# Optimization experiments

Measured on AMD Instinct MI355X. Metric: run time of the kernel, lower is better.

## Reference

```python
import jax, jax.numpy as jnp
import numpy as np

N = 50000      # nodes
E = 800000     # edges (avg degree 16)
DIN = 128
HID = 128
OUT = 10       # classes
G = 64         # graphs in batch


def setup_inputs() -> dict:
    key = jax.random.key(0)
    ks = jax.random.split(key, 10)
    x = jax.random.normal(ks[0], (N, DIN), dtype=jnp.float32)
    edge_index = jax.random.randint(ks[1], (2, E), 0, N, dtype=jnp.int32)
    edge_weight = jax.random.uniform(ks[2], (E,), dtype=jnp.float32)
    batch = jnp.sort(jax.random.randint(ks[3], (N,), 0, G, dtype=jnp.int32))
    W1 = jax.random.normal(ks[4], (DIN, HID), dtype=jnp.float32) / np.sqrt(DIN)
    b1 = jnp.zeros((HID,), dtype=jnp.float32)
    W2 = jax.random.normal(ks[5], (HID, HID), dtype=jnp.float32) / np.sqrt(HID)
    b2 = jnp.zeros((HID,), dtype=jnp.float32)
    W3 = jax.random.normal(ks[6], (HID, OUT), dtype=jnp.float32) / np.sqrt(HID)
    b3 = jnp.zeros((OUT,), dtype=jnp.float32)
    return {"x": x, "edge_index": edge_index, "edge_weight": edge_weight,
            "batch": batch, "W1": W1, "b1": b1, "W2": W2, "b2": b2,
            "W3": W3, "b3": b3}


def _gcn_norm(edge_index, edge_weight, n_nodes):
    # PyG gcn_norm: add self-loops with weight 1, D^-1/2 (A+I) D^-1/2
    loop = jnp.arange(n_nodes, dtype=edge_index.dtype)
    src = jnp.concatenate([edge_index[0], loop])
    dst = jnp.concatenate([edge_index[1], loop])
    w = jnp.concatenate([edge_weight, jnp.ones((n_nodes,), edge_weight.dtype)])
    deg = jax.ops.segment_sum(w, dst, num_segments=n_nodes)
    dinv = jnp.where(deg > 0, jax.lax.rsqrt(deg), 0.0)
    norm = dinv[src] * w * dinv[dst]
    return src, dst, norm


def _gcn_conv(x, W, b, src, dst, norm, n_nodes):
    h = x @ W                                      # [N, F] dense transform
    msg = norm[:, None] * h[src]                   # gather + scale  [E+N, F]
    out = jax.ops.segment_sum(msg, dst, num_segments=n_nodes)  # scatter-add
    return out + b


def reference(x, edge_index, edge_weight, batch, W1, b1, W2, b2, W3, b3):
    src, dst, norm = _gcn_norm(edge_index, edge_weight, N)
    h = jax.nn.relu(_gcn_conv(x, W1, b1, src, dst, norm, N))
    h = jax.nn.relu(_gcn_conv(h, W2, b2, src, dst, norm, N))
    h = _gcn_conv(h, W3, b3, src, dst, norm, N)    # [N, OUT]
    # global_mean_pool over graph ids
    sums = jax.ops.segment_sum(h, batch, num_segments=G)          # [G, OUT]
    cnts = jax.ops.segment_sum(jnp.ones((N,), h.dtype), batch, num_segments=G)
    pooled = sums / jnp.maximum(cnts, 1.0)[:, None]
    return jax.nn.log_softmax(pooled, axis=1)
```

## Files before the change

### kernel.cpp

```cpp
#include <hip/hip_runtime.h>
#include <math.h>

#define NN 50000
#define EE 800000
#define GG 64
#define FD 128
#define OUTD 10
#define GB 782
#define BB 196
#define NBU 196
#define NBK 128
#define CH 6250

typedef __attribute__((ext_vector_type(8))) short s8v;
typedef __attribute__((ext_vector_type(4))) float f4v;

static __device__ inline unsigned short f2b(float f) {
    unsigned int u = __float_as_uint(f);
    return (unsigned short)((u + 0x7FFFu + ((u >> 16) & 1u)) >> 16);
}


__global__ void k_prep(const float* __restrict__ W1, const float* __restrict__ W2,
                       unsigned short* __restrict__ Wt1, unsigned short* __restrict__ Wt2) {
    int i = blockIdx.x * blockDim.x + threadIdx.x;
    if (i < FD * FD) {
        int nn = i >> 7, k = i & 127;
        Wt1[i] = f2b(W1[k * FD + nn]);
        Wt2[i] = f2b(W2[k * FD + nn]);
    }
}


static __device__ inline void gemm_f32in_body(int bid, const float* __restrict__ A,
        const unsigned short* __restrict__ Wt, unsigned short* __restrict__ out, int n) {
    int tid = threadIdx.x;
    int wave = tid >> 6, lane = tid & 63;
    int quad = lane >> 4, c16 = lane & 15;
    int rowbase = bid * 64 + wave * 16;
    int rowA = rowbase + c16;
    if (rowA >= n) rowA = n - 1;
    f4v acc[8];
    #pragma unroll
    for (int t = 0; t < 8; ++t) acc[t] = (f4v){0.f, 0.f, 0.f, 0.f};
    #pragma unroll
    for (int k0 = 0; k0 < 128; k0 += 32) {
        const float* ap = A + (size_t)rowA * FD + k0 + quad * 8;
        float4 a0 = *(const float4*)ap;
        float4 a1 = *(const float4*)(ap + 4);
        s8v a;
        a[0] = (short)f2b(a0.x); a[1] = (short)f2b(a0.y);
        a[2] = (short)f2b(a0.z); a[3] = (short)f2b(a0.w);
        a[4] = (short)f2b(a1.x); a[5] = (short)f2b(a1.y);
        a[6] = (short)f2b(a1.z); a[7] = (short)f2b(a1.w);
        #pragma unroll
        for (int t = 0; t < 8; ++t) {
            s8v b = *(const s8v*)(Wt + (size_t)(t * 16 + c16) * FD + k0 + quad * 8);
            acc[t] = __builtin_amdgcn_mfma_f32_16x16x32_bf16(a, b, acc[t], 0, 0, 0);
        }
    }
    #pragma unroll
    for (int t = 0; t < 8; ++t) {
        #pragma unroll
        for (int r = 0; r < 4; ++r) {
            int row = rowbase + quad * 4 + r;
            if (row < n) out[(size_t)row * FD + t * 16 + c16] = f2b(acc[t][r]);
        }
    }
}

__global__ __launch_bounds__(256) void k_megaA(const float* __restrict__ x,
        const unsigned short* __restrict__ Wt1, unsigned short* __restrict__ hA,
        const int* __restrict__ dst, int* __restrict__ cnt2d,
        const int* __restrict__ batch, int* __restrict__ gstart) {
    int b = blockIdx.x;
    int tid = threadIdx.x;
    if (b < GB) {
        gemm_f32in_body(b, x, Wt1, hA, NN);
    } else if (b < GB + NBK) {
        __shared__ unsigned hist[NBU];
        int blk = b - GB;
        if (tid < NBU) hist[tid] = 0;
        __syncthreads();
        int e0 = blk * CH;
        for (int e = e0 + tid; e < e0 + CH; e += 256)
            atomicAdd(&hist[(unsigned)dst[e] >> 8], 1u);
        __syncthreads();
        if (tid < NBU) cnt2d[tid * NBK + blk] = (int)hist[tid];
    } else {
        int i = (b - GB - NBK) * 256 + tid;
        if (i < NN) {
            int bb = batch[i];
            int bp = (i == 0) ? -1 : batch[i - 1];
            for (int g = bp + 1; g <= bb; ++g) gstart[g] = i;
            if (i == NN - 1)
                for (int g = bb + 1; g <= GG; ++g) gstart[g] = NN;
        }
    }
}


__global__ __launch_bounds__(256) void k_scatter(const int* __restrict__ src,
        const int* __restrict__ dst, const float* __restrict__ ew,
        const int* __restrict__ cnt2d, int* __restrict__ bbase_g,
        uint2* __restrict__ rec) {
    __shared__ int colsum[NBU];
    __shared__ int ownoff[NBU];
    __shared__ unsigned cur[NBU];
    __shared__ int wtot_s[4];
    int tid = threadIdx.x;
    int blk = blockIdx.x;
    if (tid < NBU) {
        const int* c = cnt2d + tid * NBK;
        int own = 0, tot = 0;
        for (int b = 0; b < NBK; ++b) {
            int t = c[b];
            if (b < blk) own += t;
            tot += t;
        }
        ownoff[tid] = own;
        colsum[tid] = tot;
    }
    __syncthreads();
    {
        int lane = tid & 63, wv = tid >> 6;
        int v = (tid < NBU) ? colsum[tid] : 0;
        int s = v;
        #pragma unroll
        for (int off = 1; off < 64; off <<= 1) {
            int u = __shfl_up(s, off, 64);
            if (lane >= off) s += u;
        }
        if (lane == 63) wtot_s[wv] = s;
        __syncthreads();
        int pre = 0;
        for (int j = 0; j < wv; ++j) pre += wtot_s[j];
        int base = pre + s - v;
        if (tid < NBU) {
            cur[tid] = (unsigned)(base + ownoff[tid]);
            if (blk == 0) bbase_g[tid] = base;
        }
        if (blk == 0 && tid == NBU - 1) bbase_g[NBU] = base + v;
    }
    __syncthreads();
    int e0 = blk * CH;
    for (int e = e0 + tid; e < e0 + CH; e += 256) {
        int d = dst[e];
        unsigned bkt = (unsigned)d >> 8;
        unsigned pos = atomicAdd(&cur[bkt], 1u);
        rec[pos] = make_uint2(((unsigned)(d & 255) << 16) | (unsigned)src[e],
                              __float_as_uint(ew[e]));
    }
}


__global__ __launch_bounds__(1024) void k_rank(const uint2* __restrict__ rec,
        const int* __restrict__ bbase, unsigned short* __restrict__ rankb,
        int* __restrict__ rowptr, float* __restrict__ dinv, uint2* __restrict__ ent) {
    __shared__ unsigned cntS[256];
    __shared__ float wdegS[256];
    __shared__ int wtot_s[4];
    int b = blockIdx.x;
    int tid = threadIdx.x;
    if (tid < 256) { cntS[tid] = 0; wdegS[tid] = 0.0f; }
    __syncthreads();
    int beg = bbase[b], end = bbase[b + 1];
    for (int s = beg + tid; s < end; s += 1024) {
        uint2 r = rec[s];
        unsigned dl = r.x >> 16;
        unsigned old = atomicAdd(&cntS[dl], 1u);
        rankb[s] = (unsigned short)old;
        atomicAdd(&wdegS[dl], __uint_as_float(r.y));
    }
    __syncthreads();
    if (tid < 256) {
        int lane = tid & 63, wv = tid >> 6;
        int v = (int)cntS[tid];
        int s = v;
        #pragma unroll
        for (int off = 1; off < 64; off <<= 1) {
            int u = __shfl_up(s, off, 64);
            if (lane >= off) s += u;
        }
        if (lane == 63) wtot_s[wv] = s;
        __syncthreads();
        int pre = 0;
        for (int j = 0; j < wv; ++j) pre += wtot_s[j];
        int excl = pre + s - v;
        int node = b * 256 + tid;
        if (node < NN) {
            int r = beg + node + excl;
            rowptr[node] = r;
            float di = 1.0f / sqrtf(wdegS[tid] + 1.0f);
            dinv[node] = di;
            ent[r + v] = make_uint2((unsigned)node, __float_as_uint(di * di));
        }
        if (node == NN - 1) rowptr[NN] = EE + NN;
    }
}


__global__ __launch_bounds__(1024) void k_fill2(const uint2* __restrict__ rec,
        const unsigned short* __restrict__ rankb, const int* __restrict__ bbase,
        const int* __restrict__ rowptr, const float* __restrict__ dinv,
        uint2* __restrict__ ent) {
    int b = blockIdx.x;
    int tid = threadIdx.x;
    int beg = bbase[b], end = bbase[b + 1];
    for (int s = beg + tid; s < end; s += 1024) {
        uint2 r = rec[s];
        unsigned sn = r.x & 0xFFFFu;
        int d = (b << 8) | (int)(r.x >> 16);
        int pos = rowptr[d] + (int)rankb[s];
        float val = dinv[sn] * __uint_as_float(r.y) * dinv[d];
        ent[pos] = make_uint2(sn, __float_as_uint(val));
    }
}


__global__ __launch_bounds__(256) void k_gemm_bf(const unsigned short* __restrict__ A,
        const unsigned short* __restrict__ Wt, unsigned short* __restrict__ out, int n) {
    int tid = threadIdx.x;
    int wave = tid >> 6, lane = tid & 63;
    int quad = lane >> 4, c16 = lane & 15;
    int rowbase = blockIdx.x * 64 + wave * 16;
    int rowA = rowbase + c16;
    if (rowA >= n) rowA = n - 1;
    f4v acc[8];
    #pragma unroll
    for (int t = 0; t < 8; ++t) acc[t] = (f4v){0.f, 0.f, 0.f, 0.f};
    #pragma unroll
    for (int k0 = 0; k0 < 128; k0 += 32) {
        s8v a = *(const s8v*)(A + (size_t)rowA * FD + k0 + quad * 8);
        #pragma unroll
        for (int t = 0; t < 8; ++t) {
            s8v b = *(const s8v*)(Wt + (size_t)(t * 16 + c16) * FD + k0 + quad * 8);
            acc[t] = __builtin_amdgcn_mfma_f32_16x16x32_bf16(a, b, acc[t], 0, 0, 0);
        }
    }
    #pragma unroll
    for (int t = 0; t < 8; ++t) {
        #pragma unroll
        for (int r = 0; r < 4; ++r) {
            int row = rowbase + quad * 4 + r;
            if (row < n) out[(size_t)row * FD + t * 16 + c16] = f2b(acc[t][r]);
        }
    }
}

__global__ void k_gemm10(const unsigned short* __restrict__ A, const float* __restrict__ W,
                         float* __restrict__ out, int n) {
    __shared__ float Ws[FD * OUTD];
    int tid = threadIdx.x;
    for (int i = tid; i < FD * OUTD; i += blockDim.x) Ws[i] = W[i];
    __syncthreads();
    int i = blockIdx.x * blockDim.x + tid;
    if (i >= n) return;
    float acc[OUTD];
    #pragma unroll
    for (int c = 0; c < OUTD; ++c) acc[c] = 0.0f;
    const unsigned short* a = A + (size_t)i * FD;
    for (int k0 = 0; k0 < FD; k0 += 8) {
        uint4 t = *(const uint4*)(a + k0);
        float av[8];
        av[0] = __uint_as_float(t.x << 16); av[1] = __uint_as_float(t.x & 0xFFFF0000u);
        av[2] = __uint_as_float(t.y << 16); av[3] = __uint_as_float(t.y & 0xFFFF0000u);
        av[4] = __uint_as_float(t.z << 16); av[5] = __uint_as_float(t.z & 0xFFFF0000u);
        av[6] = __uint_as_float(t.w << 16); av[7] = __uint_as_float(t.w & 0xFFFF0000u);
        #pragma unroll
        for (int j = 0; j < 8; ++j)
            #pragma unroll
            for (int c = 0; c < OUTD; ++c) acc[c] += av[j] * Ws[(k0 + j) * OUTD + c];
    }
    float* o = out + (size_t)i * OUTD;
    #pragma unroll
    for (int c = 0; c < OUTD; ++c) o[c] = acc[c];
}

__global__ __launch_bounds__(256) void k_spmm_bf(const int* __restrict__ rowptr,
        const uint2* __restrict__ ent, const unsigned short* __restrict__ tin,
        const float* __restrict__ bias, unsigned short* __restrict__ out,
        int n, int dorelu) {
    int w = (blockIdx.x * blockDim.x + threadIdx.x) >> 6;
    int lane = threadIdx.x & 63;
    if (w >= n) return;
    int c = lane & 15, g = lane >> 4;
    int beg = rowptr[w], end = rowptr[w + 1];
    float acc[8];
    #pragma unroll
    for (int j = 0; j < 8; ++j) acc[j] = 0.0f;
    int e0 = beg;
    for (; e0 + 16 <= end; e0 += 16) {
        uint2 en[4];
        uint4 t[4];
        #pragma unroll
        for (int u = 0; u < 4; ++u) en[u] = ent[e0 + 4 * u + g];
        #pragma unroll
        for (int u = 0; u < 4; ++u)
            t[u] = *(const uint4*)(tin + (size_t)en[u].x * FD + c * 8);
        #pragma unroll
        for (int u = 0; u < 4; ++u) {
            float v = __uint_as_float(en[u].y);
            acc[0] += v * __uint_as_float(t[u].x << 16);
            acc[1] += v * __uint_as_float(t[u].x & 0xFFFF0000u);
            acc[2] += v * __uint_as_float(t[u].y << 16);
            acc[3] += v * __uint_as_float(t[u].y & 0xFFFF0000u);
            acc[4] += v * __uint_as_float(t[u].z << 16);
            acc[5] += v * __uint_as_float(t[u].z & 0xFFFF0000u);
            acc[6] += v * __uint_as_float(t[u].w << 16);
            acc[7] += v * __uint_as_float(t[u].w & 0xFFFF0000u);
        }
    }
    for (; e0 < end; e0 += 4) {
        int e = e0 + g;
        uint2 en = (e < end) ? ent[e] : make_uint2(0u, 0u);
        float v = (e < end) ? __uint_as_float(en.y) : 0.0f;
        uint4 t = *(const uint4*)(tin + (size_t)en.x * FD + c * 8);
        acc[0] += v * __uint_as_float(t.x << 16);
        acc[1] += v * __uint_as_float(t.x & 0xFFFF0000u);
        acc[2] += v * __uint_as_float(t.y << 16);
        acc[3] += v * __uint_as_float(t.y & 0xFFFF0000u);
        acc[4] += v * __uint_as_float(t.z << 16);
        acc[5] += v * __uint_as_float(t.z & 0xFFFF0000u);
        acc[6] += v * __uint_as_float(t.w << 16);
        acc[7] += v * __uint_as_float(t.w & 0xFFFF0000u);
    }
    #pragma unroll
    for (int j = 0; j < 8; ++j) {
        acc[j] += __shfl_xor(acc[j], 16, 64);
        acc[j] += __shfl_xor(acc[j], 32, 64);
    }
    if (g == 0) {
        uint4 r;
        float o[8];
        #pragma unroll
        for (int j = 0; j < 8; ++j) {
            float x = acc[j] + bias[c * 8 + j];
            o[j] = dorelu ? fmaxf(x, 0.0f) : x;
        }
        r.x = (unsigned)f2b(o[0]) | ((unsigned)f2b(o[1]) << 16);
        r.y = (unsigned)f2b(o[2]) | ((unsigned)f2b(o[3]) << 16);
        r.z = (unsigned)f2b(o[4]) | ((unsigned)f2b(o[5]) << 16);
        r.w = (unsigned)f2b(o[6]) | ((unsigned)f2b(o[7]) << 16);
        *(uint4*)(out + (size_t)w * FD + c * 8) = r;
    }
}

__global__ void k_spmm10(const int* __restrict__ rowptr, const uint2* __restrict__ ent,
        const float* __restrict__ tin, const float* __restrict__ bias,
        float* __restrict__ out, int n) {
    int t = blockIdx.x * blockDim.x + threadIdx.x;
    int node = t / OUTD;
    int c = t - node * OUTD;
    if (node >= n) return;
    int beg = rowptr[node], end = rowptr[node + 1];
    float acc = 0.0f;
    for (int e = beg; e < end; ++e) {
        uint2 en = ent[e];
        acc += __uint_as_float(en.y) * tin[(size_t)en.x * OUTD + c];
    }
    out[(size_t)node * OUTD + c] = acc + bias[c];
}


__global__ __launch_bounds__(256) void k_poolfin(const float* __restrict__ h,
        const int* __restrict__ gstart, float* __restrict__ out) {
    int g = blockIdx.x;
    int beg = gstart[g], end = gstart[g + 1];
    int tid = threadIdx.x;
    int lane = tid & 63, wv = tid >> 6;
    float acc[OUTD];
    #pragma unroll
    for (int c = 0; c < OUTD; ++c) acc[c] = 0.0f;
    for (int i = beg + tid; i < end; i += 256) {
        const float* hp = h + (size_t)i * OUTD;
        #pragma unroll
        for (int c = 0; c < OUTD; ++c) acc[c] += hp[c];
    }
    #pragma unroll
    for (int off = 32; off >= 1; off >>= 1)
        #pragma unroll
        for (int c = 0; c < OUTD; ++c) acc[c] += __shfl_down(acc[c], off, 64);
    __shared__ float ws[4][OUTD];
    if (lane == 0)
        #pragma unroll
        for (int c = 0; c < OUTD; ++c) ws[wv][c] = acc[c];
    __syncthreads();
    if (tid == 0) {
        float cf = fmaxf((float)(end - beg), 1.0f);
        float v[OUTD], m = -1e30f;
        #pragma unroll
        for (int c = 0; c < OUTD; ++c) {
            v[c] = (ws[0][c] + ws[1][c] + ws[2][c] + ws[3][c]) / cf;
            m = fmaxf(m, v[c]);
        }
        float s = 0.0f;
        #pragma unroll
        for (int c = 0; c < OUTD; ++c) s += expf(v[c] - m);
        float l = logf(s);
        #pragma unroll
        for (int c = 0; c < OUTD; ++c) out[g * OUTD + c] = v[c] - m - l;
    }
}


extern "C" void kernel_launch(void* const* d_in, const int* in_sizes, int n_in,
                              void* d_out, int out_size, void* d_ws, size_t ws_size,
                              hipStream_t stream) {
    const float* x   = (const float*)d_in[0];
    const int*   ei  = (const int*)d_in[1];
    const float* ew  = (const float*)d_in[2];
    const int*   bat = (const int*)d_in[3];
    const float* W1  = (const float*)d_in[4];
    const float* b1  = (const float*)d_in[5];
    const float* W2  = (const float*)d_in[6];
    const float* b2  = (const float*)d_in[7];
    const float* W3  = (const float*)d_in[8];
    const float* b3  = (const float*)d_in[9];
    float* out = (float*)d_out;

    const int* src = ei;
    const int* dst = ei + EE;

    char* p = (char*)d_ws;
    auto alloc = [&](size_t bytes) -> void* {
        void* r = (void*)p;
        p += (bytes + 255) & ~(size_t)255;
        return r;
    };
    int*            cnt2d  = (int*)  alloc((size_t)NBU * NBK * 4);
    int*            bbase  = (int*)  alloc((size_t)(NBU + 1) * 4);
    uint2*          rec    = (uint2*)alloc((size_t)EE * 8);
    unsigned short* rankb  = (unsigned short*)alloc((size_t)EE * 2);
    float*          dinv   = (float*)alloc((size_t)NN * 4);
    int*            rowptr = (int*)  alloc((size_t)(NN + 1) * 4);
    uint2*          ent    = (uint2*)alloc((size_t)(EE + NN) * 8);
    unsigned short* Wt1    = (unsigned short*)alloc((size_t)FD * FD * 2);
    unsigned short* Wt2    = (unsigned short*)alloc((size_t)FD * FD * 2);
    unsigned short* hA     = (unsigned short*)alloc((size_t)NN * FD * 2);
    unsigned short* hB     = (unsigned short*)alloc((size_t)NN * FD * 2);
    float*          bufC   = (float*)alloc((size_t)NN * OUTD * 4);
    float*          bufD   = (float*)alloc((size_t)NN * OUTD * 4);
    int*            gstart = (int*)  alloc((size_t)(GG + 1) * 4);
    (void)ws_size; (void)in_sizes; (void)n_in; (void)out_size;

    const int B = 256;
    k_prep   <<<(FD * FD + B - 1) / B, B, 0, stream>>>(W1, W2, Wt1, Wt2);
    k_megaA  <<<GB + NBK + BB, B, 0, stream>>>(x, Wt1, hA, dst, cnt2d, bat, gstart);
    k_scatter<<<NBK, B, 0, stream>>>(src, dst, ew, cnt2d, bbase, rec);
    k_rank   <<<NBU, 1024, 0, stream>>>(rec, bbase, rankb, rowptr, dinv, ent);
    k_fill2  <<<NBU, 1024, 0, stream>>>(rec, rankb, bbase, rowptr, dinv, ent);

    k_spmm_bf<<<(NN * 64 + B - 1) / B, B, 0, stream>>>(rowptr, ent, hA, b1, hB, NN, 1);
    k_gemm_bf<<<GB, B, 0, stream>>>(hB, Wt2, hA, NN);
    k_spmm_bf<<<(NN * 64 + B - 1) / B, B, 0, stream>>>(rowptr, ent, hA, b2, hB, NN, 1);
    k_gemm10 <<<(NN + B - 1) / B, B, 0, stream>>>(hB, W3, bufC, NN);
    k_spmm10 <<<(NN * OUTD + B - 1) / B, B, 0, stream>>>(rowptr, ent, bufC, b3, bufD, NN);
    k_poolfin<<<GG, 256, 0, stream>>>(bufD, gstart, out);
}
```

Baseline: 268.2 us.

## Fuse rank/fill CSR build and fold W3 projection into second SpMM

Merges the rank and fill kernels into one kernel that keeps edge records and ranks in registers (up to RCAP per thread) and uses shared-memory row offsets and dst dinv. This avoids a second pass over rec and the global rowptr/dinv lookups. The source-side dinv factor is no longer baked into edge values and is instead applied at SpMM time through an extra gather. The layer-2 SpMM now applies bias, ReLU and the 128x10 W3 projection in registers, which removes the separate gemm10 pass and the bf16 hidden write and read. The trade-off is an extra dinv gather per edge in every SpMM and more register pressure in the fused kernels.

```diff
diff --git a/kernel.cpp b/kernel.cpp
--- a/kernel.cpp
+++ b/kernel.cpp
@@ -11,6 +11,7 @@
 #define NBU 196
 #define NBK 128
 #define CH 6250
+#define RCAP 8
 
 typedef __attribute__((ext_vector_type(8))) short s8v;
 typedef __attribute__((ext_vector_type(4))) float f4v;
@@ -154,66 +155,87 @@
 }
 
 
-__global__ __launch_bounds__(1024) void k_rank(const uint2* __restrict__ rec,
-        const int* __restrict__ bbase, unsigned short* __restrict__ rankb,
-        int* __restrict__ rowptr, float* __restrict__ dinv, uint2* __restrict__ ent) {
+__global__ __launch_bounds__(1024) void k_rankfill(const uint2* __restrict__ rec,
+        const int* __restrict__ bbase, int* __restrict__ rowptr, float* __restrict__ dinv_g,
+        uint2* __restrict__ ent, unsigned short* __restrict__ rankb) {
     __shared__ unsigned cntS[256];
     __shared__ float wdegS[256];
     __shared__ int wtot_s[4];
+    __shared__ int rowS[256];
+    __shared__ float dinvS[256];
     int b = blockIdx.x;
     int tid = threadIdx.x;
     if (tid < 256) { cntS[tid] = 0; wdegS[tid] = 0.0f; }
     __syncthreads();
     int beg = bbase[b], end = bbase[b + 1];
-    for (int s = beg + tid; s < end; s += 1024) {
+    int s0 = beg + tid;
+    uint2 rv[RCAP];
+    unsigned rk[RCAP];
+    #pragma unroll
+    for (int k = 0; k < RCAP; ++k) {
+        int s = s0 + k * 1024;
+        if (s < end) {
+            uint2 r = rec[s];
+            unsigned dl = r.x >> 16;
+            unsigned old = atomicAdd(&cntS[dl], 1u);
+            atomicAdd(&wdegS[dl], __uint_as_float(r.y));
+            rv[k] = r; rk[k] = old;
+        }
+    }
+    for (int s = s0 + RCAP * 1024; s < end; s += 1024) {
         uint2 r = rec[s];
         unsigned dl = r.x >> 16;
         unsigned old = atomicAdd(&cntS[dl], 1u);
+        atomicAdd(&wdegS[dl], __uint_as_float(r.y));
         rankb[s] = (unsigned short)old;
-        atomicAdd(&wdegS[dl], __uint_as_float(r.y));
-    }
-    __syncthreads();
-    if (tid < 256) {
+    }
+    __syncthreads();
+    {
         int lane = tid & 63, wv = tid >> 6;
-        int v = (int)cntS[tid];
+        int v = (tid < 256) ? (int)cntS[tid] : 0;
         int s = v;
         #pragma unroll
         for (int off = 1; off < 64; off <<= 1) {
             int u = __shfl_up(s, off, 64);
             if (lane >= off) s += u;
         }
-        if (lane == 63) wtot_s[wv] = s;
+        if (tid < 256 && lane == 63) wtot_s[wv] = s;
         __syncthreads();
-        int pre = 0;
-        for (int j = 0; j < wv; ++j) pre += wtot_s[j];
-        int excl = pre + s - v;
-        int node = b * 256 + tid;
-        if (node < NN) {
-            int r = beg + node + excl;
-            rowptr[node] = r;
-            float di = 1.0f / sqrtf(wdegS[tid] + 1.0f);
-            dinv[node] = di;
-            ent[r + v] = make_uint2((unsigned)node, __float_as_uint(di * di));
-        }
-        if (node == NN - 1) rowptr[NN] = EE + NN;
-    }
-}
-
-
-__global__ __launch_bounds__(1024) void k_fill2(const uint2* __restrict__ rec,
-        const unsigned short* __restrict__ rankb, const int* __restrict__ bbase,
-        const int* __restrict__ rowptr, const float* __restrict__ dinv,
-        uint2* __restrict__ ent) {
-    int b = blockIdx.x;
-    int tid = threadIdx.x;
-    int beg = bbase[b], end = bbase[b + 1];
-    for (int s = beg + tid; s < end; s += 1024) {
+        if (tid < 256) {
+            int pre = 0;
+            for (int j = 0; j < wv; ++j) pre += wtot_s[j];
+            int excl = pre + s - v;
+            int node = b * 256 + tid;
+            if (node < NN) {
+                int r = beg + node + excl;
+                rowS[tid] = r;
+                rowptr[node] = r;
+                float di = 1.0f / sqrtf(wdegS[tid] + 1.0f);
+                dinvS[tid] = di;
+                dinv_g[node] = di;
+                ent[r + v] = make_uint2((unsigned)node, __float_as_uint(di));
+            }
+            if (node == NN - 1) rowptr[NN] = EE + NN;
+        }
+    }
+    __syncthreads();
+    #pragma unroll
+    for (int k = 0; k < RCAP; ++k) {
+        int s = s0 + k * 1024;
+        if (s < end) {
+            uint2 r = rv[k];
+            unsigned dl = r.x >> 16;
+            int pos = rowS[dl] + (int)rk[k];
+            float val = __uint_as_float(r.y) * dinvS[dl];
+            ent[pos] = make_uint2(r.x & 0xFFFFu, __float_as_uint(val));
+        }
+    }
+    for (int s = s0 + RCAP * 1024; s < end; s += 1024) {
         uint2 r = rec[s];
-        unsigned sn = r.x & 0xFFFFu;
-        int d = (b << 8) | (int)(r.x >> 16);
-        int pos = rowptr[d] + (int)rankb[s];
-        float val = dinv[sn] * __uint_as_float(r.y) * dinv[d];
-        ent[pos] = make_uint2(sn, __float_as_uint(val));
+        unsigned dl = r.x >> 16;
+        int pos = rowS[dl] + (int)rankb[s];
+        float val = __uint_as_float(r.y) * dinvS[dl];
+        ent[pos] = make_uint2(r.x & 0xFFFFu, __float_as_uint(val));
     }
 }
 
@@ -248,39 +270,11 @@
     }
 }
 
-__global__ void k_gemm10(const unsigned short* __restrict__ A, const float* __restrict__ W,
-                         float* __restrict__ out, int n) {
-    __shared__ float Ws[FD * OUTD];
-    int tid = threadIdx.x;
-    for (int i = tid; i < FD * OUTD; i += blockDim.x) Ws[i] = W[i];
-    __syncthreads();
-    int i = blockIdx.x * blockDim.x + tid;
-    if (i >= n) return;
-    float acc[OUTD];
-    #pragma unroll
-    for (int c = 0; c < OUTD; ++c) acc[c] = 0.0f;
-    const unsigned short* a = A + (size_t)i * FD;
-    for (int k0 = 0; k0 < FD; k0 += 8) {
-        uint4 t = *(const uint4*)(a + k0);
-        float av[8];
-        av[0] = __uint_as_float(t.x << 16); av[1] = __uint_as_float(t.x & 0xFFFF0000u);
-        av[2] = __uint_as_float(t.y << 16); av[3] = __uint_as_float(t.y & 0xFFFF0000u);
-        av[4] = __uint_as_float(t.z << 16); av[5] = __uint_as_float(t.z & 0xFFFF0000u);
-        av[6] = __uint_as_float(t.w << 16); av[7] = __uint_as_float(t.w & 0xFFFF0000u);
-        #pragma unroll
-        for (int j = 0; j < 8; ++j)
-            #pragma unroll
-            for (int c = 0; c < OUTD; ++c) acc[c] += av[j] * Ws[(k0 + j) * OUTD + c];
-    }
-    float* o = out + (size_t)i * OUTD;
-    #pragma unroll
-    for (int c = 0; c < OUTD; ++c) o[c] = acc[c];
-}
 
 __global__ __launch_bounds__(256) void k_spmm_bf(const int* __restrict__ rowptr,
-        const uint2* __restrict__ ent, const unsigned short* __restrict__ tin,
-        const float* __restrict__ bias, unsigned short* __restrict__ out,
-        int n, int dorelu) {
+        const uint2* __restrict__ ent, const float* __restrict__ dinv,
+        const unsigned short* __restrict__ tin, const float* __restrict__ bias,
+        unsigned short* __restrict__ out, int n, int dorelu) {
     int w = (blockIdx.x * blockDim.x + threadIdx.x) >> 6;
     int lane = threadIdx.x & 63;
     if (w >= n) return;
@@ -292,15 +286,18 @@
     int e0 = beg;
     for (; e0 + 16 <= end; e0 += 16) {
         uint2 en[4];
+        float dv[4];
         uint4 t[4];
         #pragma unroll
         for (int u = 0; u < 4; ++u) en[u] = ent[e0 + 4 * u + g];
+        #pragma unroll
+        for (int u = 0; u < 4; ++u) dv[u] = dinv[en[u].x];
         #pragma unroll
         for (int u = 0; u < 4; ++u)
             t[u] = *(const uint4*)(tin + (size_t)en[u].x * FD + c * 8);
         #pragma unroll
         for (int u = 0; u < 4; ++u) {
-            float v = __uint_as_float(en[u].y);
+            float v = __uint_as_float(en[u].y) * dv[u];
             acc[0] += v * __uint_as_float(t[u].x << 16);
             acc[1] += v * __uint_as_float(t[u].x & 0xFFFF0000u);
             acc[2] += v * __uint_as_float(t[u].y << 16);
@@ -314,7 +311,7 @@
     for (; e0 < end; e0 += 4) {
         int e = e0 + g;
         uint2 en = (e < end) ? ent[e] : make_uint2(0u, 0u);
-        float v = (e < end) ? __uint_as_float(en.y) : 0.0f;
+        float v = (e < end) ? __uint_as_float(en.y) * dinv[en.x] : 0.0f;
         uint4 t = *(const uint4*)(tin + (size_t)en.x * FD + c * 8);
         acc[0] += v * __uint_as_float(t.x << 16);
         acc[1] += v * __uint_as_float(t.x & 0xFFFF0000u);
@@ -346,9 +343,98 @@
     }
 }
 
+__global__ __launch_bounds__(256) void k_spmm_w3(const int* __restrict__ rowptr,
+        const uint2* __restrict__ ent, const float* __restrict__ dinv,
+        const unsigned short* __restrict__ tin, const float* __restrict__ bias2,
+        const float* __restrict__ W3, float* __restrict__ outc, int n) {
+    __shared__ float Ws3[FD * 11];
+    __shared__ float Bs2[FD];
+    int tid = threadIdx.x;
+    for (int i = tid; i < FD * OUTD; i += 256)
+        Ws3[(i / OUTD) * 11 + (i % OUTD)] = W3[i];
+    if (tid < FD) Bs2[tid] = bias2[tid];
+    __syncthreads();
+    int w = (blockIdx.x * blockDim.x + tid) >> 6;
+    int lane = tid & 63;
+    if (w >= n) return;
+    int c = lane & 15, g = lane >> 4;
+    int beg = rowptr[w], end = rowptr[w + 1];
+    float acc[8];
+    #pragma unroll
+    for (int j = 0; j < 8; ++j) acc[j] = 0.0f;
+    int e0 = beg;
+    for (; e0 + 16 <= end; e0 += 16) {
+        uint2 en[4];
+        float dv[4];
+        uint4 t[4];
+        #pragma unroll
+        for (int u = 0; u < 4; ++u) en[u] = ent[e0 + 4 * u + g];
+        #pragma unroll
+        for (int u = 0; u < 4; ++u) dv[u] = dinv[en[u].x];
+        #pragma unroll
+        for (int u = 0; u < 4; ++u)
+            t[u] = *(const uint4*)(tin + (size_t)en[u].x * FD + c * 8);
+        #pragma unroll
+        for (int u = 0; u < 4; ++u) {
+            float v = __uint_as_float(en[u].y) * dv[u];
+            acc[0] += v * __uint_as_float(t[u].x << 16);
+            acc[1] += v * __uint_as_float(t[u].x & 0xFFFF0000u);
+            acc[2] += v * __uint_as_float(t[u].y << 16);
+            acc[3] += v * __uint_as_float(t[u].y & 0xFFFF0000u);
+            acc[4] += v * __uint_as_float(t[u].z << 16);
+            acc[5] += v * __uint_as_float(t[u].z & 0xFFFF0000u);
+            acc[6] += v * __uint_as_float(t[u].w << 16);
+            acc[7] += v * __uint_as_float(t[u].w & 0xFFFF0000u);
+        }
+    }
+    for (; e0 < end; e0 += 4) {
+        int e = e0 + g;
+        uint2 en = (e < end) ? ent[e] : make_uint2(0u, 0u);
+        float v = (e < end) ? __uint_as_float(en.y) * dinv[en.x] : 0.0f;
+        uint4 t = *(const uint4*)(tin + (size_t)en.x * FD + c * 8);
+        acc[0] += v * __uint_as_float(t.x << 16);
+        acc[1] += v * __uint_as_float(t.x & 0xFFFF0000u);
+        acc[2] += v * __uint_as_float(t.y << 16);
+        acc[3] += v * __uint_as_float(t.y & 0xFFFF0000u);
+        acc[4] += v * __uint_as_float(t.z << 16);
+        acc[5] += v * __uint_as_float(t.z & 0xFFFF0000u);
+        acc[6] += v * __uint_as_float(t.w << 16);
+        acc[7] += v * __uint_as_float(t.w & 0xFFFF0000u);
+    }
+    #pragma unroll
+    for (int j = 0; j < 8; ++j) {
+        acc[j] += __shfl_xor(acc[j], 16, 64);
+        acc[j] += __shfl_xor(acc[j], 32, 64);
+    }
+    float o[8];
+    #pragma unroll
+    for (int j = 0; j < 8; ++j)
+        o[j] = fmaxf(acc[j] + Bs2[c * 8 + j], 0.0f);
+    float p0 = 0.0f, p1 = 0.0f, p2 = 0.0f;
+    #pragma unroll
+    for (int j = 0; j < 8; ++j) {
+        const float* wr = &Ws3[(c * 8 + j) * 11 + g];
+        p0 += o[j] * wr[0];
+        p1 += o[j] * wr[4];
+        if (g < 2) p2 += o[j] * wr[8];
+    }
+    #pragma unroll
+    for (int off = 1; off < 16; off <<= 1) {
+        p0 += __shfl_xor(p0, off, 64);
+        p1 += __shfl_xor(p1, off, 64);
+        p2 += __shfl_xor(p2, off, 64);
+    }
+    if (c == 0) {
+        float* op = outc + (size_t)w * OUTD;
+        op[g] = p0;
+        op[g + 4] = p1;
+        if (g < 2) op[g + 8] = p2;
+    }
+}
+
 __global__ void k_spmm10(const int* __restrict__ rowptr, const uint2* __restrict__ ent,
-        const float* __restrict__ tin, const float* __restrict__ bias,
-        float* __restrict__ out, int n) {
+        const float* __restrict__ dinv, const float* __restrict__ tin,
+        const float* __restrict__ bias, float* __restrict__ out, int n) {
     int t = blockIdx.x * blockDim.x + threadIdx.x;
     int node = t / OUTD;
     int c = t - node * OUTD;
@@ -357,7 +443,7 @@
     float acc = 0.0f;
     for (int e = beg; e < end; ++e) {
         uint2 en = ent[e];
-        acc += __uint_as_float(en.y) * tin[(size_t)en.x * OUTD + c];
+        acc += __uint_as_float(en.y) * dinv[en.x] * tin[(size_t)en.x * OUTD + c];
     }
     out[(size_t)node * OUTD + c] = acc + bias[c];
 }
@@ -445,16 +531,14 @@
     (void)ws_size; (void)in_sizes; (void)n_in; (void)out_size;
 
     const int B = 256;
-    k_prep   <<<(FD * FD + B - 1) / B, B, 0, stream>>>(W1, W2, Wt1, Wt2);
-    k_megaA  <<<GB + NBK + BB, B, 0, stream>>>(x, Wt1, hA, dst, cnt2d, bat, gstart);
-    k_scatter<<<NBK, B, 0, stream>>>(src, dst, ew, cnt2d, bbase, rec);
-    k_rank   <<<NBU, 1024, 0, stream>>>(rec, bbase, rankb, rowptr, dinv, ent);
-    k_fill2  <<<NBU, 1024, 0, stream>>>(rec, rankb, bbase, rowptr, dinv, ent);
-
-    k_spmm_bf<<<(NN * 64 + B - 1) / B, B, 0, stream>>>(rowptr, ent, hA, b1, hB, NN, 1);
-    k_gemm_bf<<<GB, B, 0, stream>>>(hB, Wt2, hA, NN);
-    k_spmm_bf<<<(NN * 64 + B - 1) / B, B, 0, stream>>>(rowptr, ent, hA, b2, hB, NN, 1);
-    k_gemm10 <<<(NN + B - 1) / B, B, 0, stream>>>(hB, W3, bufC, NN);
-    k_spmm10 <<<(NN * OUTD + B - 1) / B, B, 0, stream>>>(rowptr, ent, bufC, b3, bufD, NN);
-    k_poolfin<<<GG, 256, 0, stream>>>(bufD, gstart, out);
-}
+    k_prep    <<<(FD * FD + B - 1) / B, B, 0, stream>>>(W1, W2, Wt1, Wt2);
+    k_megaA   <<<GB + NBK + BB, B, 0, stream>>>(x, Wt1, hA, dst, cnt2d, bat, gstart);
+    k_scatter <<<NBK, B, 0, stream>>>(src, dst, ew, cnt2d, bbase, rec);
+    k_rankfill<<<NBU, 1024, 0, stream>>>(rec, bbase, rowptr, dinv, ent, rankb);
+
+    k_spmm_bf <<<(NN * 64 + B - 1) / B, B, 0, stream>>>(rowptr, ent, dinv, hA, b1, hB, NN, 1);
+    k_gemm_bf <<<GB, B, 0, stream>>>(hB, Wt2, hA, NN);
+    k_spmm_w3 <<<(NN * 64 + B - 1) / B, B, 0, stream>>>(rowptr, ent, dinv, hA, b2, W3, bufC, NN);
+    k_spmm10  <<<(NN * OUTD + B - 1) / B, B, 0, stream>>>(rowptr, ent, dinv, bufC, b3, bufD, NN);
+    k_poolfin <<<GG, 256, 0, stream>>>(bufD, gstart, out);
+}
```

After: 279.2 us. +4.1%, slower.
